# Kernel optimization log

Hardware: AMD Instinct MI355X
Metric: run time of the kernel (lower is better)

The kernel has to match this reference:

```python
import jax, jax.numpy as jnp
import numpy as np

B, S, D, H, E = 8, 196, 768, 12, 8
HD = D // H  # 64
FF = 4 * D   # 3072
EPS = 1e-5


def setup_inputs() -> dict:
    key = jax.random.key(0)
    ks = jax.random.split(key, 12)
    s = 0.02
    inp = {
        'x': jax.random.normal(ks[0], (B, S, D), jnp.float32),
        'ln1_g': jnp.ones((D,), jnp.float32),
        'ln1_b': jnp.zeros((D,), jnp.float32),
        'Wq': jax.random.normal(ks[1], (D, D), jnp.float32) * s,
        'bq': jnp.zeros((D,), jnp.float32),
        'Wk': jax.random.normal(ks[2], (D, HD), jnp.float32) * s,
        'bk': jnp.zeros((HD,), jnp.float32),
        'Wv': jax.random.normal(ks[3], (D, HD), jnp.float32) * s,
        'bv': jnp.zeros((HD,), jnp.float32),
        'ln2_g': jnp.ones((D,), jnp.float32),
        'ln2_b': jnp.zeros((D,), jnp.float32),
        'Wg': jax.random.normal(ks[4], (D, E), jnp.float32) * s,
        'bg': jnp.zeros((E,), jnp.float32),
        'W1': jax.random.normal(ks[5], (E, D, FF), jnp.float32) * s,
        'b1': jnp.zeros((E, FF), jnp.float32),
        'W2': jax.random.normal(ks[6], (E, FF, D), jnp.float32) * s,
        'b2': jnp.zeros((E, D), jnp.float32),
    }
    return inp


def _layernorm(x, g, b):
    mu = jnp.mean(x, axis=-1, keepdims=True)
    var = jnp.var(x, axis=-1, keepdims=True)
    return (x - mu) * jax.lax.rsqrt(var + EPS) * g + b


def _rotate_half(x):
    x1, x2 = jnp.split(x, 2, axis=-1)
    return jnp.concatenate((-x2, x1), axis=-1)


def _rope(seq_len):
    inv_freq = 1.0 / (10000.0 ** (jnp.arange(0, HD, 2, dtype=jnp.float32) / HD))
    freqs = jnp.arange(seq_len, dtype=jnp.float32)[:, None] * inv_freq[None, :]
    emb = jnp.concatenate((freqs, freqs), axis=-1)  # [S, HD]
    return emb[None, :, None, :]  # [1, S, 1, HD]


def _attention(x, Wq, bq, Wk, bk, Wv, bv):
    b, s, _ = x.shape
    q = (x @ Wq + bq).reshape(b, s, H, HD)
    k = (x @ Wk + bk).reshape(b, s, 1, HD)
    v = (x @ Wv + bv).reshape(b, s, 1, HD)
    k = jnp.broadcast_to(k, (b, s, H, HD))
    v = jnp.broadcast_to(v, (b, s, H, HD))
    pe = _rope(s)
    cos, sin = jnp.cos(pe), jnp.sin(pe)
    q = q * cos + _rotate_half(q) * sin
    k = k * cos + _rotate_half(k) * sin
    scale = HD ** -0.5
    # NOTE: faithful to source -- matmul over the last two dims of [b,s,h,d],
    # i.e. attention across HEADS, not sequence positions.
    attn = jnp.einsum('bshd,bsgd->bshg', q, k) * scale
    attn = jax.nn.softmax(attn, axis=-1)
    out = jnp.einsum('bshg,bsgd->bshd', attn, v)
    return out.reshape(b, s, H * HD)


def _moe(x, Wg, bg, W1, b1, W2, b2):
    b, s, d = x.shape
    xt = x.reshape(-1, d)  # [T, D]
    gates = jax.nn.softmax(xt @ Wg + bg, axis=-1)
    top1 = jnp.argmax(gates, axis=-1)  # topk(k=2)[:,0] == argmax
    out = jnp.zeros_like(xt)
    for e in range(E):  # small fixed expert count
        h = jax.nn.gelu(xt @ W1[e] + b1[e], approximate=False)
        y = h @ W2[e] + b2[e]
        out = jnp.where((top1 == e)[:, None], y, out)
    return out.reshape(b, s, d)


def reference(x, ln1_g, ln1_b, Wq, bq, Wk, bk, Wv, bv, ln2_g, ln2_b, Wg, bg, W1, b1, W2, b2):
    res = x
    h = _layernorm(x, ln1_g, ln1_b)
    h = _attention(h, Wq, bq, Wk, bk, Wv, bv)
    x = res + h
    res = x
    h = _layernorm(x, ln2_g, ln2_b)
    h = _moe(h, Wg, bg, W1, b1, W2, b2)
    return res + h
```

## Files before the change

### kernel.cpp

```cpp
#include <hip/hip_runtime.h>


typedef unsigned short u16;
typedef short bf16x8_t __attribute__((ext_vector_type(8)));
typedef short bf16x4_t __attribute__((ext_vector_type(4)));
typedef float f32x4_t  __attribute__((ext_vector_type(4)));

#define T_TOK 1568
#define DM 768
#define HD 64
#define FF 3072
#define NE 8

#define OFF_CNT   0
#define OFF_BUCK  256
#define OFF_V     (OFF_BUCK + NE*T_TOK*4)
#define OFF_H1    (OFF_V + T_TOK*HD*4)
#define OFF_H2    (OFF_H1 + T_TOK*DM*2)
#define OFF_HMID  (OFF_H2 + T_TOK*DM*2)

__device__ __forceinline__ float bf2f(u16 h) {
    unsigned u = ((unsigned)h) << 16;
    return __builtin_bit_cast(float, u);
}
__device__ __forceinline__ u16 f2bf(float f) {
    unsigned u = __builtin_bit_cast(unsigned, f);
    unsigned r = (u + 0x7FFFu + ((u >> 16) & 1u)) >> 16;
    return (u16)r;
}
__device__ __forceinline__ float gelu_f(float x) {
    return 0.5f * x * (1.0f + erff(x * 0.70710678118654752440f));
}

__global__ __launch_bounds__(256) void k_ln1(const float* __restrict__ x,
                                             const float* __restrict__ g,
                                             const float* __restrict__ b,
                                             u16* __restrict__ h1) {
    int t = blockIdx.x, tid = threadIdx.x;
    const float* xr = x + (size_t)t * DM;
    float v0 = xr[tid], v1 = xr[tid + 256], v2 = xr[tid + 512];
    float s = v0 + v1 + v2;
#pragma unroll
    for (int m = 1; m < 64; m <<= 1) s += __shfl_xor(s, m);
    __shared__ float wr1[4], wr2[4];
    int lane = tid & 63, w = tid >> 6;
    if (lane == 0) wr1[w] = s;
    __syncthreads();
    float mu = (wr1[0] + wr1[1] + wr1[2] + wr1[3]) * (1.0f / DM);
    float d0 = v0 - mu, d1 = v1 - mu, d2 = v2 - mu;
    float vs = d0 * d0 + d1 * d1 + d2 * d2;
#pragma unroll
    for (int m = 1; m < 64; m <<= 1) vs += __shfl_xor(vs, m);
    if (lane == 0) wr2[w] = vs;
    __syncthreads();
    float var = (wr2[0] + wr2[1] + wr2[2] + wr2[3]) * (1.0f / DM);
    float rs = rsqrtf(var + 1e-5f);
    u16* hr = h1 + (size_t)t * DM;
    hr[tid]       = f2bf(d0 * rs * g[tid]       + b[tid]);
    hr[tid + 256] = f2bf(d1 * rs * g[tid + 256] + b[tid + 256]);
    hr[tid + 512] = f2bf(d2 * rs * g[tid + 512] + b[tid + 512]);
}

__global__ __launch_bounds__(256) void k_vproj(const u16* __restrict__ h1,
                                               const float* __restrict__ Wv,
                                               const float* __restrict__ bv,
                                               float* __restrict__ vout) {
    __shared__ __align__(16) u16 h1s[8 * DM];
    __shared__ float ps[4 * 8 * 64];
    int tid = threadIdx.x, tb = blockIdx.x * 8;
#pragma unroll
    for (int j = 0; j < 3; j++) {
        int cid = tid + 256 * j;
        int row = cid / 96, c = cid % 96;
        *(bf16x8_t*)&h1s[row * DM + c * 8] =
            *(const bf16x8_t*)&h1[(size_t)(tb + row) * DM + c * 8];
    }
    __syncthreads();
    int j = tid & 63, w = tid >> 6;
    float acc[8];
#pragma unroll
    for (int tt = 0; tt < 8; tt++) acc[tt] = 0.0f;
    const float* wp = Wv + (size_t)(w * 192) * HD + j;
    for (int kk = 0; kk < 192; kk += 4) {
        float w0 = wp[(size_t)(kk + 0) * HD];
        float w1 = wp[(size_t)(kk + 1) * HD];
        float w2 = wp[(size_t)(kk + 2) * HD];
        float w3 = wp[(size_t)(kk + 3) * HD];
        int kb = w * 192 + kk;
#pragma unroll
        for (int tt = 0; tt < 8; tt++) {
            bf16x4_t hh = *(const bf16x4_t*)&h1s[tt * DM + kb];
            acc[tt] += bf2f((u16)hh[0]) * w0 + bf2f((u16)hh[1]) * w1 +
                       bf2f((u16)hh[2]) * w2 + bf2f((u16)hh[3]) * w3;
        }
    }
#pragma unroll
    for (int tt = 0; tt < 8; tt++) ps[(w * 8 + tt) * 64 + j] = acc[tt];
    __syncthreads();
    int tg = tid >> 6;
#pragma unroll
    for (int s2 = 0; s2 < 2; s2++) {
        int tt = tg * 2 + s2;
        float v = ps[tt * 64 + j] + ps[(8 + tt) * 64 + j] +
                  ps[(16 + tt) * 64 + j] + ps[(24 + tt) * 64 + j] + bv[j];
        vout[(size_t)(tb + tt) * HD + j] = v;
    }
}

__global__ __launch_bounds__(256) void k_x2ln2gate(
        const float* __restrict__ x, const float* __restrict__ vws,
        const float* __restrict__ g2, const float* __restrict__ b2g,
        const float* __restrict__ Wg, const float* __restrict__ bg,
        const float* __restrict__ b2moe,
        u16* __restrict__ h2, float* __restrict__ out,
        int* __restrict__ cnt, int* __restrict__ buck) {
    __shared__ float wgs[NE * DM];
    __shared__ float g2s[DM], b2s[DM];
    int tid = threadIdx.x, tb = blockIdx.x * 8;
    for (int idx = tid; idx < NE * DM; idx += 256) {
        int e = idx / DM, c = idx % DM;
        wgs[idx] = Wg[(size_t)c * NE + e];
    }
    for (int idx = tid; idx < DM; idx += 256) { g2s[idx] = g2[idx]; b2s[idx] = b2g[idx]; }
    __syncthreads();
    int lane = tid & 63, w = tid >> 6;
    for (int ttl = 0; ttl < 2; ttl++) {
        int t = tb + w * 2 + ttl;
        float vl = vws[(size_t)t * HD + lane];
        const float* xp = x + (size_t)t * DM;
        float xv[12];
        float s = 0.0f;
#pragma unroll
        for (int i = 0; i < 12; i++) {
            float q = xp[lane + 64 * i] + vl;
            xv[i] = q; s += q;
        }
#pragma unroll
        for (int m = 1; m < 64; m <<= 1) s += __shfl_xor(s, m);
        float mu = s * (1.0f / DM);
        float vs = 0.0f;
#pragma unroll
        for (int i = 0; i < 12; i++) { float d = xv[i] - mu; vs += d * d; }
#pragma unroll
        for (int m = 1; m < 64; m <<= 1) vs += __shfl_xor(vs, m);
        float rs = rsqrtf(vs * (1.0f / DM) + 1e-5f);
        float le[NE];
#pragma unroll
        for (int e = 0; e < NE; e++) le[e] = 0.0f;
        u16* h2p = h2 + (size_t)t * DM;
#pragma unroll
        for (int i = 0; i < 12; i++) {
            int c = lane + 64 * i;
            float h = (xv[i] - mu) * rs * g2s[c] + b2s[c];
            h2p[c] = f2bf(h);
#pragma unroll
            for (int e = 0; e < NE; e++) le[e] += h * wgs[e * DM + c];
        }
#pragma unroll
        for (int e = 0; e < NE; e++) {
#pragma unroll
            for (int m = 1; m < 64; m <<= 1) le[e] += __shfl_xor(le[e], m);
        }
        float best = le[0] + bg[0]; int be = 0;
#pragma unroll
        for (int e = 1; e < NE; e++) {
            float q = le[e] + bg[e];
            if (q > best) { best = q; be = e; }
        }
        if (lane == 0) {
            int pos = atomicAdd(&cnt[be], 1);
            buck[be * T_TOK + pos] = t;
        }
        float* op = out + (size_t)t * DM;
        const float* bp = b2moe + (size_t)be * DM;
#pragma unroll
        for (int i = 0; i < 12; i++) {
            int c = lane + 64 * i;
            op[c] = xv[i] + bp[c];
        }
    }
}

__global__ __launch_bounds__(256, 2) void k_moe_gemm1(
        const u16* __restrict__ h2, const float* __restrict__ W1,
        const float* __restrict__ b1, const int* __restrict__ cnt,
        const int* __restrict__ buck, u16* __restrict__ hmid) {
    int nt = blockIdx.x, e = blockIdx.y, mt = blockIdx.z;
    int cnte = cnt[e];
    int m0 = mt * 128;
    if (m0 >= cnte) return;
    int n0 = nt * 64;
    const float* W1e = W1 + (size_t)e * DM * FF;
    __shared__ __align__(16) u16 As[128 * 72];
    __shared__ __align__(16) u16 Bs[64 * 72];
    int tid = threadIdx.x, lane = tid & 63, wid = tid >> 6;

    int arow = tid >> 3, ac = tid & 7;
    int atok[4];
#pragma unroll
    for (int j = 0; j < 4; j++) {
        int i = m0 + arow + 32 * j;
        atok[j] = (i < cnte) ? buck[e * T_TOK + i] : -1;
    }
    int bn = tid & 63, bkg = tid >> 6;

    f32x4_t acc[2][4];
#pragma unroll
    for (int mi = 0; mi < 2; mi++)
#pragma unroll
        for (int ni = 0; ni < 4; ni++) acc[mi][ni] = (f32x4_t){0.f, 0.f, 0.f, 0.f};

    bf16x8_t a_pre[4];
    float b_pre[16];
#pragma unroll
    for (int j = 0; j < 4; j++) {
        bf16x8_t v = {0, 0, 0, 0, 0, 0, 0, 0};
        if (atok[j] >= 0) v = *(const bf16x8_t*)&h2[(size_t)atok[j] * DM + ac * 8];
        a_pre[j] = v;
    }
    {
        const float* bp = W1e + (size_t)(bkg * 16) * FF + n0 + bn;
#pragma unroll
        for (int kk = 0; kk < 16; kk++) b_pre[kk] = bp[(size_t)kk * FF];
    }

    const int NK = DM / 64;
    for (int kt = 0; kt < NK; kt++) {
        __syncthreads();
#pragma unroll
        for (int j = 0; j < 4; j++)
            *(bf16x8_t*)&As[(arow + 32 * j) * 72 + ac * 8] = a_pre[j];
        {
            bf16x8_t p0, p1;
#pragma unroll
            for (int kk = 0; kk < 8; kk++) {
                p0[kk] = (short)f2bf(b_pre[kk]);
                p1[kk] = (short)f2bf(b_pre[kk + 8]);
            }
            *(bf16x8_t*)&Bs[bn * 72 + bkg * 16] = p0;
            *(bf16x8_t*)&Bs[bn * 72 + bkg * 16 + 8] = p1;
        }
        __syncthreads();
        if (kt + 1 < NK) {
            int k0 = (kt + 1) * 64;
#pragma unroll
            for (int j = 0; j < 4; j++) {
                bf16x8_t v = {0, 0, 0, 0, 0, 0, 0, 0};
                if (atok[j] >= 0)
                    v = *(const bf16x8_t*)&h2[(size_t)atok[j] * DM + k0 + ac * 8];
                a_pre[j] = v;
            }
            const float* bp = W1e + (size_t)(k0 + bkg * 16) * FF + n0 + bn;
#pragma unroll
            for (int kk = 0; kk < 16; kk++) b_pre[kk] = bp[(size_t)kk * FF];
        }
        int lr = lane & 15, q = lane >> 4;
#pragma unroll
        for (int s = 0; s < 2; s++) {
            bf16x8_t af[2], bfr[4];
#pragma unroll
            for (int mi = 0; mi < 2; mi++)
                af[mi] = *(const bf16x8_t*)&As[(wid * 32 + mi * 16 + lr) * 72 + s * 32 + q * 8];
#pragma unroll
            for (int ni = 0; ni < 4; ni++)
                bfr[ni] = *(const bf16x8_t*)&Bs[(ni * 16 + lr) * 72 + s * 32 + q * 8];
#pragma unroll
            for (int mi = 0; mi < 2; mi++)
#pragma unroll
                for (int ni = 0; ni < 4; ni++)
                    acc[mi][ni] = __builtin_amdgcn_mfma_f32_16x16x32_bf16(
                        af[mi], bfr[ni], acc[mi][ni], 0, 0, 0);
        }
    }
    int lr = lane & 15, q = lane >> 4;
    float bias[4];
#pragma unroll
    for (int ni = 0; ni < 4; ni++) bias[ni] = b1[(size_t)e * FF + n0 + ni * 16 + lr];
#pragma unroll
    for (int mi = 0; mi < 2; mi++) {
#pragma unroll
        for (int r = 0; r < 4; r++) {
            int i = m0 + wid * 32 + mi * 16 + q * 4 + r;
            if (i < cnte) {
                int t = buck[e * T_TOK + i];
                size_t base = (size_t)t * FF + n0;
#pragma unroll
                for (int ni = 0; ni < 4; ni++) {
                    float vv = acc[mi][ni][r] + bias[ni];
                    hmid[base + ni * 16 + lr] = f2bf(gelu_f(vv));
                }
            }
        }
    }
}

__global__ __launch_bounds__(256, 2) void k_moe_gemm2(
        const u16* __restrict__ hmid, const float* __restrict__ W2,
        const int* __restrict__ cnt, const int* __restrict__ buck,
        float* __restrict__ out) {
    int nt = blockIdx.x, e = blockIdx.y, z = blockIdx.z;
    int kc = z & 3, mt = z >> 2;
    int cnte = cnt[e];
    int m0 = mt * 128;
    if (m0 >= cnte) return;
    int n0 = nt * 64;
    int kbase = kc * (FF / 4);
    const float* W2e = W2 + (size_t)e * FF * DM;
    __shared__ __align__(16) u16 As[128 * 72];
    __shared__ __align__(16) u16 Bs[64 * 72];
    int tid = threadIdx.x, lane = tid & 63, wid = tid >> 6;

    int arow = tid >> 3, ac = tid & 7;
    int atok[4];
#pragma unroll
    for (int j = 0; j < 4; j++) {
        int i = m0 + arow + 32 * j;
        atok[j] = (i < cnte) ? buck[e * T_TOK + i] : -1;
    }
    int bn = tid & 63, bkg = tid >> 6;

    f32x4_t acc[2][4];
#pragma unroll
    for (int mi = 0; mi < 2; mi++)
#pragma unroll
        for (int ni = 0; ni < 4; ni++) acc[mi][ni] = (f32x4_t){0.f, 0.f, 0.f, 0.f};

    bf16x8_t a_pre[4];
    float b_pre[16];
#pragma unroll
    for (int j = 0; j < 4; j++) {
        bf16x8_t v = {0, 0, 0, 0, 0, 0, 0, 0};
        if (atok[j] >= 0)
            v = *(const bf16x8_t*)&hmid[(size_t)atok[j] * FF + kbase + ac * 8];
        a_pre[j] = v;
    }
    {
        const float* bp = W2e + (size_t)(kbase + bkg * 16) * DM + n0 + bn;
#pragma unroll
        for (int kk = 0; kk < 16; kk++) b_pre[kk] = bp[(size_t)kk * DM];
    }

    const int NK = (FF / 4) / 64;
    for (int kt = 0; kt < NK; kt++) {
        __syncthreads();
#pragma unroll
        for (int j = 0; j < 4; j++)
            *(bf16x8_t*)&As[(arow + 32 * j) * 72 + ac * 8] = a_pre[j];
        {
            bf16x8_t p0, p1;
#pragma unroll
            for (int kk = 0; kk < 8; kk++) {
                p0[kk] = (short)f2bf(b_pre[kk]);
                p1[kk] = (short)f2bf(b_pre[kk + 8]);
            }
            *(bf16x8_t*)&Bs[bn * 72 + bkg * 16] = p0;
            *(bf16x8_t*)&Bs[bn * 72 + bkg * 16 + 8] = p1;
        }
        __syncthreads();
        if (kt + 1 < NK) {
            int k0 = kbase + (kt + 1) * 64;
#pragma unroll
            for (int j = 0; j < 4; j++) {
                bf16x8_t v = {0, 0, 0, 0, 0, 0, 0, 0};
                if (atok[j] >= 0)
                    v = *(const bf16x8_t*)&hmid[(size_t)atok[j] * FF + k0 + ac * 8];
                a_pre[j] = v;
            }
            const float* bp = W2e + (size_t)(k0 + bkg * 16) * DM + n0 + bn;
#pragma unroll
            for (int kk = 0; kk < 16; kk++) b_pre[kk] = bp[(size_t)kk * DM];
        }
        int lr = lane & 15, q = lane >> 4;
#pragma unroll
        for (int s = 0; s < 2; s++) {
            bf16x8_t af[2], bfr[4];
#pragma unroll
            for (int mi = 0; mi < 2; mi++)
                af[mi] = *(const bf16x8_t*)&As[(wid * 32 + mi * 16 + lr) * 72 + s * 32 + q * 8];
#pragma unroll
            for (int ni = 0; ni < 4; ni++)
                bfr[ni] = *(const bf16x8_t*)&Bs[(ni * 16 + lr) * 72 + s * 32 + q * 8];
#pragma unroll
            for (int mi = 0; mi < 2; mi++)
#pragma unroll
                for (int ni = 0; ni < 4; ni++)
                    acc[mi][ni] = __builtin_amdgcn_mfma_f32_16x16x32_bf16(
                        af[mi], bfr[ni], acc[mi][ni], 0, 0, 0);
        }
    }
    int lr = lane & 15, q = lane >> 4;
#pragma unroll
    for (int mi = 0; mi < 2; mi++) {
#pragma unroll
        for (int r = 0; r < 4; r++) {
            int i = m0 + wid * 32 + mi * 16 + q * 4 + r;
            if (i < cnte) {
                int t = buck[e * T_TOK + i];
                size_t base = (size_t)t * DM + n0;
#pragma unroll
                for (int ni = 0; ni < 4; ni++)
                    atomicAdd(&out[base + ni * 16 + lr], acc[mi][ni][r]);
            }
        }
    }
}

extern "C" void kernel_launch(void* const* d_in, const int* in_sizes, int n_in,
                              void* d_out, int out_size, void* d_ws, size_t ws_size,
                              hipStream_t stream) {
    const float* x    = (const float*)d_in[0];
    const float* ln1g = (const float*)d_in[1];
    const float* ln1b = (const float*)d_in[2];
    const float* Wv   = (const float*)d_in[7];
    const float* bv   = (const float*)d_in[8];
    const float* ln2g = (const float*)d_in[9];
    const float* ln2b = (const float*)d_in[10];
    const float* Wg   = (const float*)d_in[11];
    const float* bg   = (const float*)d_in[12];
    const float* W1   = (const float*)d_in[13];
    const float* b1   = (const float*)d_in[14];
    const float* W2   = (const float*)d_in[15];
    const float* b2   = (const float*)d_in[16];

    char* ws = (char*)d_ws;
    int*   cnt  = (int*)(ws + OFF_CNT);
    int*   buck = (int*)(ws + OFF_BUCK);
    float* vws  = (float*)(ws + OFF_V);
    u16*   h1   = (u16*)(ws + OFF_H1);
    u16*   h2   = (u16*)(ws + OFF_H2);
    u16*   hmid = (u16*)(ws + OFF_HMID);
    float* out  = (float*)d_out;

    hipMemsetAsync(cnt, 0, NE * sizeof(int), stream);
    k_ln1<<<T_TOK, 256, 0, stream>>>(x, ln1g, ln1b, h1);
    k_vproj<<<T_TOK / 8, 256, 0, stream>>>(h1, Wv, bv, vws);
    k_x2ln2gate<<<T_TOK / 8, 256, 0, stream>>>(x, vws, ln2g, ln2b, Wg, bg, b2,
                                               h2, out, cnt, buck);
    k_moe_gemm1<<<dim3(FF / 64, NE, 13), 256, 0, stream>>>(h2, W1, b1, cnt, buck, hmid);
    k_moe_gemm2<<<dim3(DM / 64, NE, 52), 256, 0, stream>>>(hmid, W2, cnt, buck, out);
}
```

Baseline: 298.4 us.

## Fuse LN1, V-projection and LN2/gating into one kernel; double-buffer MoE GEMMs

Merges the LN1, V-projection and x2/LN2/gate kernels into a single front kernel that keeps the normalized activations in fp32 shared memory, removing two launches and the h1/v workspace round trips. Both MoE GEMMs now use a two-stage register prefetch (ping-pong buffers, unrolled by two) with the K-loop trip count hardcoded to 12. Launch-bounds occupancy is raised from 2 to 3 blocks per SIMD, and the float-to-bf16 conversion now uses the library intrinsic. Risks include extra register pressure from the doubled prefetch buffers under the tighter occupancy bound, and heavier shared-memory use in the fused front kernel.

Measured after the change: 276.7 us. -7.3%, faster.

```diff
diff --git a/kernel.cpp b/kernel.cpp
--- a/kernel.cpp
+++ b/kernel.cpp
@@ -1,9 +1,9 @@
 #include <hip/hip_runtime.h>
+#include <hip/hip_bf16.h>
 
 
 typedef unsigned short u16;
 typedef short bf16x8_t __attribute__((ext_vector_type(8)));
-typedef short bf16x4_t __attribute__((ext_vector_type(4)));
 typedef float f32x4_t  __attribute__((ext_vector_type(4)));
 
 #define T_TOK 1568
@@ -14,127 +14,102 @@
 
 #define OFF_CNT   0
 #define OFF_BUCK  256
-#define OFF_V     (OFF_BUCK + NE*T_TOK*4)
-#define OFF_H1    (OFF_V + T_TOK*HD*4)
-#define OFF_H2    (OFF_H1 + T_TOK*DM*2)
+#define OFF_H2    (OFF_BUCK + NE*T_TOK*4)
 #define OFF_HMID  (OFF_H2 + T_TOK*DM*2)
 
-__device__ __forceinline__ float bf2f(u16 h) {
-    unsigned u = ((unsigned)h) << 16;
-    return __builtin_bit_cast(float, u);
-}
 __device__ __forceinline__ u16 f2bf(float f) {
-    unsigned u = __builtin_bit_cast(unsigned, f);
-    unsigned r = (u + 0x7FFFu + ((u >> 16) & 1u)) >> 16;
-    return (u16)r;
+    return __builtin_bit_cast(u16, __float2bfloat16(f));
 }
 __device__ __forceinline__ float gelu_f(float x) {
     return 0.5f * x * (1.0f + erff(x * 0.70710678118654752440f));
 }
 
-__global__ __launch_bounds__(256) void k_ln1(const float* __restrict__ x,
-                                             const float* __restrict__ g,
-                                             const float* __restrict__ b,
-                                             u16* __restrict__ h1) {
-    int t = blockIdx.x, tid = threadIdx.x;
-    const float* xr = x + (size_t)t * DM;
-    float v0 = xr[tid], v1 = xr[tid + 256], v2 = xr[tid + 512];
-    float s = v0 + v1 + v2;
-#pragma unroll
-    for (int m = 1; m < 64; m <<= 1) s += __shfl_xor(s, m);
-    __shared__ float wr1[4], wr2[4];
-    int lane = tid & 63, w = tid >> 6;
-    if (lane == 0) wr1[w] = s;
-    __syncthreads();
-    float mu = (wr1[0] + wr1[1] + wr1[2] + wr1[3]) * (1.0f / DM);
-    float d0 = v0 - mu, d1 = v1 - mu, d2 = v2 - mu;
-    float vs = d0 * d0 + d1 * d1 + d2 * d2;
-#pragma unroll
-    for (int m = 1; m < 64; m <<= 1) vs += __shfl_xor(vs, m);
-    if (lane == 0) wr2[w] = vs;
-    __syncthreads();
-    float var = (wr2[0] + wr2[1] + wr2[2] + wr2[3]) * (1.0f / DM);
-    float rs = rsqrtf(var + 1e-5f);
-    u16* hr = h1 + (size_t)t * DM;
-    hr[tid]       = f2bf(d0 * rs * g[tid]       + b[tid]);
-    hr[tid + 256] = f2bf(d1 * rs * g[tid + 256] + b[tid + 256]);
-    hr[tid + 512] = f2bf(d2 * rs * g[tid + 512] + b[tid + 512]);
-}
-
-__global__ __launch_bounds__(256) void k_vproj(const u16* __restrict__ h1,
-                                               const float* __restrict__ Wv,
-                                               const float* __restrict__ bv,
-                                               float* __restrict__ vout) {
-    __shared__ __align__(16) u16 h1s[8 * DM];
-    __shared__ float ps[4 * 8 * 64];
-    int tid = threadIdx.x, tb = blockIdx.x * 8;
-#pragma unroll
-    for (int j = 0; j < 3; j++) {
-        int cid = tid + 256 * j;
-        int row = cid / 96, c = cid % 96;
-        *(bf16x8_t*)&h1s[row * DM + c * 8] =
-            *(const bf16x8_t*)&h1[(size_t)(tb + row) * DM + c * 8];
-    }
-    __syncthreads();
-    int j = tid & 63, w = tid >> 6;
-    float acc[8];
-#pragma unroll
-    for (int tt = 0; tt < 8; tt++) acc[tt] = 0.0f;
-    const float* wp = Wv + (size_t)(w * 192) * HD + j;
-    for (int kk = 0; kk < 192; kk += 4) {
-        float w0 = wp[(size_t)(kk + 0) * HD];
-        float w1 = wp[(size_t)(kk + 1) * HD];
-        float w2 = wp[(size_t)(kk + 2) * HD];
-        float w3 = wp[(size_t)(kk + 3) * HD];
-        int kb = w * 192 + kk;
-#pragma unroll
-        for (int tt = 0; tt < 8; tt++) {
-            bf16x4_t hh = *(const bf16x4_t*)&h1s[tt * DM + kb];
-            acc[tt] += bf2f((u16)hh[0]) * w0 + bf2f((u16)hh[1]) * w1 +
-                       bf2f((u16)hh[2]) * w2 + bf2f((u16)hh[3]) * w3;
-        }
-    }
-#pragma unroll
-    for (int tt = 0; tt < 8; tt++) ps[(w * 8 + tt) * 64 + j] = acc[tt];
-    __syncthreads();
-    int tg = tid >> 6;
-#pragma unroll
-    for (int s2 = 0; s2 < 2; s2++) {
-        int tt = tg * 2 + s2;
-        float v = ps[tt * 64 + j] + ps[(8 + tt) * 64 + j] +
-                  ps[(16 + tt) * 64 + j] + ps[(24 + tt) * 64 + j] + bv[j];
-        vout[(size_t)(tb + tt) * HD + j] = v;
-    }
-}
-
-__global__ __launch_bounds__(256) void k_x2ln2gate(
-        const float* __restrict__ x, const float* __restrict__ vws,
+__global__ __launch_bounds__(256) void k_front(
+        const float* __restrict__ x,
+        const float* __restrict__ g1, const float* __restrict__ b1,
+        const float* __restrict__ Wv, const float* __restrict__ bv,
         const float* __restrict__ g2, const float* __restrict__ b2g,
         const float* __restrict__ Wg, const float* __restrict__ bg,
         const float* __restrict__ b2moe,
         u16* __restrict__ h2, float* __restrict__ out,
         int* __restrict__ cnt, int* __restrict__ buck) {
+    __shared__ float h1s[8 * DM];
+    __shared__ float ps[4 * 8 * 64];
     __shared__ float wgs[NE * DM];
     __shared__ float g2s[DM], b2s[DM];
     int tid = threadIdx.x, tb = blockIdx.x * 8;
+    int lane = tid & 63, w = tid >> 6;
+
     for (int idx = tid; idx < NE * DM; idx += 256) {
         int e = idx / DM, c = idx % DM;
         wgs[idx] = Wg[(size_t)c * NE + e];
     }
     for (int idx = tid; idx < DM; idx += 256) { g2s[idx] = g2[idx]; b2s[idx] = b2g[idx]; }
-    __syncthreads();
-    int lane = tid & 63, w = tid >> 6;
+
+    float xa[2][12];
+#pragma unroll
     for (int ttl = 0; ttl < 2; ttl++) {
         int t = tb + w * 2 + ttl;
-        float vl = vws[(size_t)t * HD + lane];
         const float* xp = x + (size_t)t * DM;
+        float s = 0.0f;
+#pragma unroll
+        for (int i = 0; i < 12; i++) { float q = xp[lane + 64 * i]; xa[ttl][i] = q; s += q; }
+#pragma unroll
+        for (int m = 1; m < 64; m <<= 1) s += __shfl_xor(s, m);
+        float mu = s * (1.0f / DM);
+        float vs = 0.0f;
+#pragma unroll
+        for (int i = 0; i < 12; i++) { float d = xa[ttl][i] - mu; vs += d * d; }
+#pragma unroll
+        for (int m = 1; m < 64; m <<= 1) vs += __shfl_xor(vs, m);
+        float rs = rsqrtf(vs * (1.0f / DM) + 1e-5f);
+        float* hp = h1s + (size_t)(w * 2 + ttl) * DM;
+#pragma unroll
+        for (int i = 0; i < 12; i++) {
+            int c = lane + 64 * i;
+            hp[c] = (xa[ttl][i] - mu) * rs * g1[c] + b1[c];
+        }
+    }
+    __syncthreads();
+
+    {
+        float acc[8];
+#pragma unroll
+        for (int tt = 0; tt < 8; tt++) acc[tt] = 0.0f;
+        const float* wp = Wv + (size_t)(w * 192) * HD + lane;
+#pragma unroll 2
+        for (int kk = 0; kk < 192; kk += 4) {
+            float w0 = wp[(size_t)(kk + 0) * HD];
+            float w1 = wp[(size_t)(kk + 1) * HD];
+            float w2 = wp[(size_t)(kk + 2) * HD];
+            float w3 = wp[(size_t)(kk + 3) * HD];
+            int kb = w * 192 + kk;
+#pragma unroll
+            for (int tt = 0; tt < 8; tt++) {
+                f32x4_t hv = *(const f32x4_t*)&h1s[tt * DM + kb];
+                acc[tt] += hv[0] * w0 + hv[1] * w1 + hv[2] * w2 + hv[3] * w3;
+            }
+        }
+#pragma unroll
+        for (int tt = 0; tt < 8; tt++) ps[(w * 8 + tt) * 64 + lane] = acc[tt];
+    }
+    __syncthreads();
+    float vred[2];
+#pragma unroll
+    for (int s2 = 0; s2 < 2; s2++) {
+        int tt = w * 2 + s2;
+        vred[s2] = ps[tt * 64 + lane] + ps[(8 + tt) * 64 + lane] +
+                   ps[(16 + tt) * 64 + lane] + ps[(24 + tt) * 64 + lane] + bv[lane];
+    }
+
+#pragma unroll
+    for (int ttl = 0; ttl < 2; ttl++) {
+        int t = tb + w * 2 + ttl;
+        float vl = vred[ttl];
         float xv[12];
         float s = 0.0f;
 #pragma unroll
-        for (int i = 0; i < 12; i++) {
-            float q = xp[lane + 64 * i] + vl;
-            xv[i] = q; s += q;
-        }
+        for (int i = 0; i < 12; i++) { float q = xa[ttl][i] + vl; xv[i] = q; s += q; }
 #pragma unroll
         for (int m = 1; m < 64; m <<= 1) s += __shfl_xor(s, m);
         float mu = s * (1.0f / DM);
@@ -181,7 +156,7 @@
     }
 }
 
-__global__ __launch_bounds__(256, 2) void k_moe_gemm1(
+__global__ __launch_bounds__(256, 3) void k_moe_gemm1(
         const u16* __restrict__ h2, const float* __restrict__ W1,
         const float* __restrict__ b1, const int* __restrict__ cnt,
         const int* __restrict__ buck, u16* __restrict__ hmid) {
@@ -210,68 +185,72 @@
 #pragma unroll
         for (int ni = 0; ni < 4; ni++) acc[mi][ni] = (f32x4_t){0.f, 0.f, 0.f, 0.f};
 
-    bf16x8_t a_pre[4];
-    float b_pre[16];
-#pragma unroll
-    for (int j = 0; j < 4; j++) {
-        bf16x8_t v = {0, 0, 0, 0, 0, 0, 0, 0};
-        if (atok[j] >= 0) v = *(const bf16x8_t*)&h2[(size_t)atok[j] * DM + ac * 8];
-        a_pre[j] = v;
-    }
-    {
-        const float* bp = W1e + (size_t)(bkg * 16) * FF + n0 + bn;
-#pragma unroll
-        for (int kk = 0; kk < 16; kk++) b_pre[kk] = bp[(size_t)kk * FF];
-    }
-
-    const int NK = DM / 64;
-    for (int kt = 0; kt < NK; kt++) {
-        __syncthreads();
-#pragma unroll
-        for (int j = 0; j < 4; j++)
-            *(bf16x8_t*)&As[(arow + 32 * j) * 72 + ac * 8] = a_pre[j];
-        {
-            bf16x8_t p0, p1;
-#pragma unroll
-            for (int kk = 0; kk < 8; kk++) {
-                p0[kk] = (short)f2bf(b_pre[kk]);
-                p1[kk] = (short)f2bf(b_pre[kk + 8]);
-            }
-            *(bf16x8_t*)&Bs[bn * 72 + bkg * 16] = p0;
-            *(bf16x8_t*)&Bs[bn * 72 + bkg * 16 + 8] = p1;
-        }
-        __syncthreads();
-        if (kt + 1 < NK) {
-            int k0 = (kt + 1) * 64;
-#pragma unroll
-            for (int j = 0; j < 4; j++) {
-                bf16x8_t v = {0, 0, 0, 0, 0, 0, 0, 0};
-                if (atok[j] >= 0)
-                    v = *(const bf16x8_t*)&h2[(size_t)atok[j] * DM + k0 + ac * 8];
-                a_pre[j] = v;
-            }
-            const float* bp = W1e + (size_t)(k0 + bkg * 16) * FF + n0 + bn;
-#pragma unroll
-            for (int kk = 0; kk < 16; kk++) b_pre[kk] = bp[(size_t)kk * FF];
-        }
-        int lr = lane & 15, q = lane >> 4;
-#pragma unroll
-        for (int s = 0; s < 2; s++) {
-            bf16x8_t af[2], bfr[4];
-#pragma unroll
-            for (int mi = 0; mi < 2; mi++)
-                af[mi] = *(const bf16x8_t*)&As[(wid * 32 + mi * 16 + lr) * 72 + s * 32 + q * 8];
-#pragma unroll
-            for (int ni = 0; ni < 4; ni++)
-                bfr[ni] = *(const bf16x8_t*)&Bs[(ni * 16 + lr) * 72 + s * 32 + q * 8];
-#pragma unroll
-            for (int mi = 0; mi < 2; mi++)
-#pragma unroll
-                for (int ni = 0; ni < 4; ni++)
-                    acc[mi][ni] = __builtin_amdgcn_mfma_f32_16x16x32_bf16(
-                        af[mi], bfr[ni], acc[mi][ni], 0, 0, 0);
-        }
-    }
+    bf16x8_t aP[4], aQ[4];
+    float bP[16], bQ[16];
+
+#define G_LOAD(SA, SB, KT) { \
+    int k0_ = (KT) * 64; \
+    _Pragma("unroll") \
+    for (int j = 0; j < 4; j++) { \
+        bf16x8_t v_ = {0, 0, 0, 0, 0, 0, 0, 0}; \
+        if (atok[j] >= 0) v_ = *(const bf16x8_t*)&h2[(size_t)atok[j] * DM + k0_ + ac * 8]; \
+        SA[j] = v_; \
+    } \
+    const float* bp_ = W1e + (size_t)(k0_ + bkg * 16) * FF + n0 + bn; \
+    _Pragma("unroll") \
+    for (int kk = 0; kk < 16; kk++) SB[kk] = bp_[(size_t)kk * FF]; \
+}
+#define STORE_LDS(SA, SB) { \
+    _Pragma("unroll") \
+    for (int j = 0; j < 4; j++) \
+        *(bf16x8_t*)&As[(arow + 32 * j) * 72 + ac * 8] = SA[j]; \
+    bf16x8_t p0_, p1_; \
+    _Pragma("unroll") \
+    for (int kk = 0; kk < 8; kk++) { \
+        p0_[kk] = (short)f2bf(SB[kk]); \
+        p1_[kk] = (short)f2bf(SB[kk + 8]); \
+    } \
+    *(bf16x8_t*)&Bs[bn * 72 + bkg * 16] = p0_; \
+    *(bf16x8_t*)&Bs[bn * 72 + bkg * 16 + 8] = p1_; \
+}
+#define MFMA_TILE() { \
+    int lr_ = lane & 15, q_ = lane >> 4; \
+    _Pragma("unroll") \
+    for (int s = 0; s < 2; s++) { \
+        bf16x8_t af[2], bfr[4]; \
+        _Pragma("unroll") \
+        for (int mi = 0; mi < 2; mi++) \
+            af[mi] = *(const bf16x8_t*)&As[(wid * 32 + mi * 16 + lr_) * 72 + s * 32 + q_ * 8]; \
+        _Pragma("unroll") \
+        for (int ni = 0; ni < 4; ni++) \
+            bfr[ni] = *(const bf16x8_t*)&Bs[(ni * 16 + lr_) * 72 + s * 32 + q_ * 8]; \
+        _Pragma("unroll") \
+        for (int mi = 0; mi < 2; mi++) \
+            _Pragma("unroll") \
+            for (int ni = 0; ni < 4; ni++) \
+                acc[mi][ni] = __builtin_amdgcn_mfma_f32_16x16x32_bf16( \
+                    af[mi], bfr[ni], acc[mi][ni], 0, 0, 0); \
+    } \
+}
+
+    G_LOAD(aP, bP, 0)
+    G_LOAD(aQ, bQ, 1)
+    for (int kt = 0; kt < 12; kt += 2) {
+        __syncthreads();
+        STORE_LDS(aP, bP)
+        __syncthreads();
+        if (kt + 2 < 12) G_LOAD(aP, bP, kt + 2)
+        MFMA_TILE()
+        __syncthreads();
+        STORE_LDS(aQ, bQ)
+        __syncthreads();
+        if (kt + 3 < 12) G_LOAD(aQ, bQ, kt + 3)
+        MFMA_TILE()
+    }
+#undef G_LOAD
+#undef STORE_LDS
+#undef MFMA_TILE
+
     int lr = lane & 15, q = lane >> 4;
     float bias[4];
 #pragma unroll
@@ -294,7 +273,7 @@
     }
 }
 
-__global__ __launch_bounds__(256, 2) void k_moe_gemm2(
+__global__ __launch_bounds__(256, 3) void k_moe_gemm2(
         const u16* __restrict__ hmid, const float* __restrict__ W2,
         const int* __restrict__ cnt, const int* __restrict__ buck,
         float* __restrict__ out) {
@@ -325,69 +304,72 @@
 #pragma unroll
         for (int ni = 0; ni < 4; ni++) acc[mi][ni] = (f32x4_t){0.f, 0.f, 0.f, 0.f};
 
-    bf16x8_t a_pre[4];
-    float b_pre[16];
-#pragma unroll
-    for (int j = 0; j < 4; j++) {
-        bf16x8_t v = {0, 0, 0, 0, 0, 0, 0, 0};
-        if (atok[j] >= 0)
-            v = *(const bf16x8_t*)&hmid[(size_t)atok[j] * FF + kbase + ac * 8];
-        a_pre[j] = v;
-    }
-    {
-        const float* bp = W2e + (size_t)(kbase + bkg * 16) * DM + n0 + bn;
-#pragma unroll
-        for (int kk = 0; kk < 16; kk++) b_pre[kk] = bp[(size_t)kk * DM];
-    }
-
-    const int NK = (FF / 4) / 64;
-    for (int kt = 0; kt < NK; kt++) {
-        __syncthreads();
-#pragma unroll
-        for (int j = 0; j < 4; j++)
-            *(bf16x8_t*)&As[(arow + 32 * j) * 72 + ac * 8] = a_pre[j];
-        {
-            bf16x8_t p0, p1;
-#pragma unroll
-            for (int kk = 0; kk < 8; kk++) {
-                p0[kk] = (short)f2bf(b_pre[kk]);
-                p1[kk] = (short)f2bf(b_pre[kk + 8]);
-            }
-            *(bf16x8_t*)&Bs[bn * 72 + bkg * 16] = p0;
-            *(bf16x8_t*)&Bs[bn * 72 + bkg * 16 + 8] = p1;
-        }
-        __syncthreads();
-        if (kt + 1 < NK) {
-            int k0 = kbase + (kt + 1) * 64;
-#pragma unroll
-            for (int j = 0; j < 4; j++) {
-                bf16x8_t v = {0, 0, 0, 0, 0, 0, 0, 0};
-                if (atok[j] >= 0)
-                    v = *(const bf16x8_t*)&hmid[(size_t)atok[j] * FF + k0 + ac * 8];
-                a_pre[j] = v;
-            }
-            const float* bp = W2e + (size_t)(k0 + bkg * 16) * DM + n0 + bn;
-#pragma unroll
-            for (int kk = 0; kk < 16; kk++) b_pre[kk] = bp[(size_t)kk * DM];
-        }
-        int lr = lane & 15, q = lane >> 4;
-#pragma unroll
-        for (int s = 0; s < 2; s++) {
-            bf16x8_t af[2], bfr[4];
-#pragma unroll
-            for (int mi = 0; mi < 2; mi++)
-                af[mi] = *(const bf16x8_t*)&As[(wid * 32 + mi * 16 + lr) * 72 + s * 32 + q * 8];
-#pragma unroll
-            for (int ni = 0; ni < 4; ni++)
-                bfr[ni] = *(const bf16x8_t*)&Bs[(ni * 16 + lr) * 72 + s * 32 + q * 8];
-#pragma unroll
-            for (int mi = 0; mi < 2; mi++)
-#pragma unroll
-                for (int ni = 0; ni < 4; ni++)
-                    acc[mi][ni] = __builtin_amdgcn_mfma_f32_16x16x32_bf16(
-                        af[mi], bfr[ni], acc[mi][ni], 0, 0, 0);
-        }
-    }
+    bf16x8_t aP[4], aQ[4];
+    float bP[16], bQ[16];
+
+#define G_LOAD(SA, SB, KT) { \
+    int k0_ = kbase + (KT) * 64; \
+    _Pragma("unroll") \
+    for (int j = 0; j < 4; j++) { \
+        bf16x8_t v_ = {0, 0, 0, 0, 0, 0, 0, 0}; \
+        if (atok[j] >= 0) v_ = *(const bf16x8_t*)&hmid[(size_t)atok[j] * FF + k0_ + ac * 8]; \
+        SA[j] = v_; \
+    } \
+    const float* bp_ = W2e + (size_t)(k0_ + bkg * 16) * DM + n0 + bn; \
+    _Pragma("unroll") \
+    for (int kk = 0; kk < 16; kk++) SB[kk] = bp_[(size_t)kk * DM]; \
+}
+#define STORE_LDS(SA, SB) { \
+    _Pragma("unroll") \
+    for (int j = 0; j < 4; j++) \
+        *(bf16x8_t*)&As[(arow + 32 * j) * 72 + ac * 8] = SA[j]; \
+    bf16x8_t p0_, p1_; \
+    _Pragma("unroll") \
+    for (int kk = 0; kk < 8; kk++) { \
+        p0_[kk] = (short)f2bf(SB[kk]); \
+        p1_[kk] = (short)f2bf(SB[kk + 8]); \
+    } \
+    *(bf16x8_t*)&Bs[bn * 72 + bkg * 16] = p0_; \
+    *(bf16x8_t*)&Bs[bn * 72 + bkg * 16 + 8] = p1_; \
+}
+#define MFMA_TILE() { \
+    int lr_ = lane & 15, q_ = lane >> 4; \
+    _Pragma("unroll") \
+    for (int s = 0; s < 2; s++) { \
+        bf16x8_t af[2], bfr[4]; \
+        _Pragma("unroll") \
+        for (int mi = 0; mi < 2; mi++) \
+            af[mi] = *(const bf16x8_t*)&As[(wid * 32 + mi * 16 + lr_) * 72 + s * 32 + q_ * 8]; \
+        _Pragma("unroll") \
+        for (int ni = 0; ni < 4; ni++) \
+            bfr[ni] = *(const bf16x8_t*)&Bs[(ni * 16 + lr_) * 72 + s * 32 + q_ * 8]; \
+        _Pragma("unroll") \
+        for (int mi = 0; mi < 2; mi++) \
+            _Pragma("unroll") \
+            for (int ni = 0; ni < 4; ni++) \
+                acc[mi][ni] = __builtin_amdgcn_mfma_f32_16x16x32_bf16( \
+                    af[mi], bfr[ni], acc[mi][ni], 0, 0, 0); \
+    } \
+}
+
+    G_LOAD(aP, bP, 0)
+    G_LOAD(aQ, bQ, 1)
+    for (int kt = 0; kt < 12; kt += 2) {
+        __syncthreads();
+        STORE_LDS(aP, bP)
+        __syncthreads();
+        if (kt + 2 < 12) G_LOAD(aP, bP, kt + 2)
+        MFMA_TILE()
+        __syncthreads();
+        STORE_LDS(aQ, bQ)
+        __syncthreads();
+        if (kt + 3 < 12) G_LOAD(aQ, bQ, kt + 3)
+        MFMA_TILE()
+    }
+#undef G_LOAD
+#undef STORE_LDS
+#undef MFMA_TILE
+
     int lr = lane & 15, q = lane >> 4;
 #pragma unroll
     for (int mi = 0; mi < 2; mi++) {
@@ -425,17 +407,13 @@
     char* ws = (char*)d_ws;
     int*   cnt  = (int*)(ws + OFF_CNT);
     int*   buck = (int*)(ws + OFF_BUCK);
-    float* vws  = (float*)(ws + OFF_V);
-    u16*   h1   = (u16*)(ws + OFF_H1);
     u16*   h2   = (u16*)(ws + OFF_H2);
     u16*   hmid = (u16*)(ws + OFF_HMID);
     float* out  = (float*)d_out;
 
     hipMemsetAsync(cnt, 0, NE * sizeof(int), stream);
-    k_ln1<<<T_TOK, 256, 0, stream>>>(x, ln1g, ln1b, h1);
-    k_vproj<<<T_TOK / 8, 256, 0, stream>>>(h1, Wv, bv, vws);
-    k_x2ln2gate<<<T_TOK / 8, 256, 0, stream>>>(x, vws, ln2g, ln2b, Wg, bg, b2,
-                                               h2, out, cnt, buck);
+    k_front<<<T_TOK / 8, 256, 0, stream>>>(x, ln1g, ln1b, Wv, bv, ln2g, ln2b,
+                                           Wg, bg, b2, h2, out, cnt, buck);
     k_moe_gemm1<<<dim3(FF / 64, NE, 13), 256, 0, stream>>>(h2, W1, b1, cnt, buck, hmid);
     k_moe_gemm2<<<dim3(DM / 64, NE, 52), 256, 0, stream>>>(hmid, W2, cnt, buck, out);
 }
```
